# Performance work log

Measured on AMD Instinct MI355X. Metric: run time of the kernel, lower is better.

Reference implementation:

```python
import jax, jax.numpy as jnp
import numpy as np

B, D, H, W, C = 8, 4, 56, 56, 128
HEADS = 4
WD, WH, WW = 2, 7, 7
SD, SH, SW = 1, 3, 3
N = WD * WH * WW            # tokens per window = 98
NW = (D // WD) * (H // WH) * (W // WW)  # windows per sample = 128
SCALE = (C // HEADS) ** -0.5
EPS = 1e-5


def _rel_pos_index():
    coords = np.stack(np.meshgrid(np.arange(WD), np.arange(WH), np.arange(WW), indexing='ij'))
    coords = coords.reshape(3, -1)                    # (3, N)
    rel = (coords[:, :, None] - coords[:, None, :]).transpose(1, 2, 0)  # (N, N, 3)
    rel[:, :, 0] += WD - 1
    rel[:, :, 1] += WH - 1
    rel[:, :, 2] += WW - 1
    rel[:, :, 0] *= (2 * WH - 1) * (2 * WW - 1)
    rel[:, :, 1] *= (2 * WW - 1)
    return rel.sum(-1)                                # (N, N) int

REL_IDX = jnp.asarray(_rel_pos_index())


def _np_window_partition(x, wd, wh, ww):
    b, d, h, w, c = x.shape
    x = x.reshape(b, d // wd, wd, h // wh, wh, w // ww, ww, c)
    return x.transpose(0, 1, 3, 5, 2, 4, 6, 7).reshape(-1, wd * wh * ww, c)


def _attn_mask():
    img = np.zeros((1, D, H, W, 1), np.float32)
    cnt = 0
    for ds in (slice(None, -WD), slice(-WD, -SD), slice(-SD, None)):
        for hs in (slice(None, -WH), slice(-WH, -SH), slice(-SH, None)):
            for ws in (slice(None, -WW), slice(-WW, -SW), slice(-SW, None)):
                img[:, ds, hs, ws, :] = cnt
                cnt += 1
    mw = _np_window_partition(img, WD, WH, WW)[..., 0]         # (nW, N)
    m = mw[:, None, :] - mw[:, :, None]                        # (nW, N, N)
    return jnp.asarray(np.where(m != 0, -100.0, 0.0).astype(np.float32))

ATTN_MASK = _attn_mask()  # (nW, N, N)


def window_partition(x):
    b = x.shape[0]
    x = x.reshape(b, D // WD, WD, H // WH, WH, W // WW, WW, C)
    return x.transpose(0, 1, 3, 5, 2, 4, 6, 7).reshape(-1, N, C)


def window_reverse(wins, b):
    x = wins.reshape(b, D // WD, H // WH, W // WW, WD, WH, WW, C)
    return x.transpose(0, 1, 4, 2, 5, 3, 6, 7).reshape(b, D, H, W, C)


def layernorm(x, g, b):
    mu = jnp.mean(x, axis=-1, keepdims=True)
    var = jnp.mean(jnp.square(x - mu), axis=-1, keepdims=True)
    return (x - mu) / jnp.sqrt(var + EPS) * g + b


def swin_block(x, norm1_g, norm1_b, qkv_w, qkv_b, rpb_table, proj_w, proj_b,
               norm2_g, norm2_b, fc1_w, fc1_b, fc2_w, fc2_b):
    shortcut = x
    h1 = layernorm(x, norm1_g, norm1_b)
    # cyclic shift (pad amounts are 0 for these dims)
    shifted = jnp.roll(h1, (-SD, -SH, -SW), axis=(1, 2, 3))
    xw = window_partition(shifted)                    # (B*nW, N, C)
    Bn = xw.shape[0]
    qkv = (xw @ qkv_w + qkv_b).reshape(Bn, N, 3, HEADS, C // HEADS)
    qkv = qkv.transpose(2, 0, 3, 1, 4)                # (3, Bn, h, N, c)
    q, k, v = qkv[0], qkv[1], qkv[2]
    attn = jnp.einsum('bhnc,bhmc->bhnm', q * SCALE, k)
    bias = rpb_table[REL_IDX].transpose(2, 0, 1)      # (h, N, N)
    attn = attn + bias[None]
    attn = attn.reshape(B, NW, HEADS, N, N) + ATTN_MASK[None, :, None]
    attn = jax.nn.softmax(attn.reshape(Bn, HEADS, N, N), axis=-1)
    out = jnp.einsum('bhnm,bhmc->bhnc', attn, v)
    out = out.transpose(0, 2, 1, 3).reshape(Bn, N, C)
    out = out @ proj_w + proj_b
    xr = window_reverse(out, B)
    xr = jnp.roll(xr, (SD, SH, SW), axis=(1, 2, 3))
    x1 = shortcut + xr
    h2 = layernorm(x1, norm2_g, norm2_b)
    mlp = jax.nn.gelu(h2 @ fc1_w + fc1_b, approximate=False) @ fc2_w + fc2_b
    return x1 + mlp


def setup_inputs() -> dict:
    key = jax.random.key(0)
    ks = jax.random.split(key, 6)
    s = 0.02
    return {
        'x': jax.random.normal(ks[0], (B, D, H, W, C), jnp.float32),
        'norm1_g': jnp.ones((C,), jnp.float32),
        'norm1_b': jnp.zeros((C,), jnp.float32),
        'qkv_w': jax.random.normal(ks[1], (C, 3 * C), jnp.float32) * s,
        'qkv_b': jnp.zeros((3 * C,), jnp.float32),
        'rpb_table': jax.random.normal(ks[2], ((2 * WD - 1) * (2 * WH - 1) * (2 * WW - 1), HEADS), jnp.float32) * s,
        'proj_w': jax.random.normal(ks[3], (C, C), jnp.float32) * s,
        'proj_b': jnp.zeros((C,), jnp.float32),
        'norm2_g': jnp.ones((C,), jnp.float32),
        'norm2_b': jnp.zeros((C,), jnp.float32),
        'fc1_w': jax.random.normal(ks[4], (C, 4 * C), jnp.float32) * s,
        'fc1_b': jnp.zeros((4 * C,), jnp.float32),
        'fc2_w': jax.random.normal(ks[5], (4 * C, C), jnp.float32) * s,
        'fc2_b': jnp.zeros((C,), jnp.float32),
    }


def reference(x, norm1_g, norm1_b, qkv_w, qkv_b, rpb_table, proj_w, proj_b,
              norm2_g, norm2_b, fc1_w, fc1_b, fc2_w, fc2_b):
    return swin_block(x, norm1_g, norm1_b, qkv_w, qkv_b, rpb_table, proj_w, proj_b,
                      norm2_g, norm2_b, fc1_w, fc1_b, fc2_w, fc2_b)
```

## Files before the change

kernel.cpp:

```cpp
#include <hip/hip_runtime.h>
#include <hip/hip_bf16.h>
#include <cstdint>
#include <cstddef>

using bf16 = __hip_bfloat16;
typedef __bf16 bf16x8 __attribute__((ext_vector_type(8)));
typedef float f32x4 __attribute__((ext_vector_type(4)));

#define DEV static __device__ __forceinline__

DEV bf16 f2b(float x) { return __float2bfloat16(x); }
DEV float b2f(bf16 x) { return __bfloat162float(x); }
DEV f32x4 mfma16(bf16x8 a, bf16x8 b, f32x4 c) {
    return __builtin_amdgcn_mfma_f32_16x16x32_bf16(a, b, c, 0, 0, 0);
}
DEV float gelu_f(float x) {
    float u2 = x * x;
    float u = x * (0.7978845608028654f + 0.0356774081363001f * u2);
    float s = 1.f / (1.f + __expf(-2.f * u));
    return x * s;
}
DEV void gload16(const bf16* g, bf16* l) {
    __builtin_amdgcn_global_load_lds(
        (const __attribute__((address_space(1))) unsigned int*)g,
        (__attribute__((address_space(3))) unsigned int*)l, 16, 0, 0);
}

constexpr int NTOK = 98;
constexpr int BNWIN = 1024;
constexpr int MTOT = BNWIN * NTOK;
constexpr float SCALE = 0.17677669529663687f;
constexpr float EPS = 1e-5f;

__global__ __launch_bounds__(256) void k_prep(const float* __restrict__ qkv_w,
        const float* __restrict__ proj_w, const float* __restrict__ fc1_w,
        const float* __restrict__ fc2_w, const float* __restrict__ rpb,
        bf16* __restrict__ QWs, bf16* __restrict__ PW,
        bf16* __restrict__ W1, bf16* __restrict__ W2, float* __restrict__ BT) {
    int tid = blockIdx.x * 256 + threadIdx.x;
    int stride = gridDim.x * 256;
    for (int i = tid; i < 384 * 128; i += stride) {
        int t = i >> 13, r = (i >> 7) & 63, kswz = i & 127;
        int k = kswz ^ ((r & 7) << 3);
        QWs[i] = f2b(qkv_w[(size_t)k * 384 + t * 64 + r]);
    }
    for (int i = tid; i < 128 * 128; i += stride) {
        int n = i >> 7, k = i & 127;
        PW[i] = f2b(proj_w[k * 128 + n]);
    }
    for (int i = tid; i < 512 * 128; i += stride) {
        int t = i >> 13, r = (i >> 7) & 63, kswz = i & 127;
        int k = kswz ^ ((r & 7) << 3);
        W1[i] = f2b(fc1_w[(size_t)k * 512 + t * 64 + r]);
    }
    for (int i = tid; i < 512 * 128; i += stride) {
        int t = i >> 13, c = (i >> 6) & 127, kswz = i & 63;
        int kk = kswz ^ ((c & 7) << 3);
        W2[i] = f2b(fc2_w[(size_t)(t * 64 + kk) * 128 + c]);
    }
    for (int i = tid; i < 4 * 98 * 98; i += stride) {
        int h = i / 9604, r = i - h * 9604;
        int ii = r / 98, jj = r - ii * 98;
        int di = ii >= 49, ri = ii - di * 49, hi = ri / 7, wi = ri - hi * 7;
        int dj = jj >= 49, rj = jj - dj * 49, hj = rj / 7, wj = rj - hj * 7;
        int bidx = (di - dj + 1) * 169 + (hi - hj + 6) * 13 + (wi - wj + 6);
        BT[i] = rpb[bidx * 4 + h];
    }
}

__global__ __launch_bounds__(256) void k_qkvln(const float* __restrict__ x,
        const float* __restrict__ g, const float* __restrict__ be,
        const bf16* __restrict__ QWs, const float* __restrict__ bias,
        bf16* __restrict__ out) {
    __shared__ __align__(16) bf16 As[64 * 136];
    __shared__ __align__(16) bf16 Bt[64 * 128];
    int tid = threadIdx.x;
    int row0 = blockIdx.x * 64;
    int wave = tid >> 6, lane = tid & 63;
    int lrow = lane & 15, kg8 = (lane >> 4) * 8, g4 = (lane >> 4) * 4;
    int swzq = (lrow & 7) << 3;

    #pragma unroll
    for (int p = 0; p < 4; ++p) {
        int vi = tid + p * 256;
        int row = vi >> 4, cg = vi & 15;
        int r = row0 + row;
        int bn = r / 98, n = r - bn * 98;
        int b = bn >> 7, wr = bn & 127;
        int dB = wr >> 6, hB = (wr >> 3) & 7, wB = wr & 7;
        int dd = (n >= 49), rem = n - dd * 49;
        int hh = rem / 7, ww = rem - hh * 7;
        int dp = dB * 2 + dd, hp = hB * 7 + hh, wp = wB * 7 + ww;
        int ds = (dp + 1) & 3;
        int hs = hp + 3; if (hs >= 56) hs -= 56;
        int wsv = wp + 3; if (wsv >= 56) wsv -= 56;
        size_t src = ((size_t)((b * 4 + ds) * 56 + hs) * 56 + wsv) * 128 + cg * 8;
        float4 v0 = *(const float4*)&x[src];
        float4 v1 = *(const float4*)&x[src + 4];
        float s = v0.x + v0.y + v0.z + v0.w + v1.x + v1.y + v1.z + v1.w;
        float sq = v0.x*v0.x + v0.y*v0.y + v0.z*v0.z + v0.w*v0.w
                 + v1.x*v1.x + v1.y*v1.y + v1.z*v1.z + v1.w*v1.w;
        #pragma unroll
        for (int m = 1; m < 16; m <<= 1) { s += __shfl_xor(s, m); sq += __shfl_xor(sq, m); }
        float mean = s * (1.f / 128.f);
        float var = sq * (1.f / 128.f) - mean * mean;
        float rstd = rsqrtf(var + EPS);
        float4 g0 = *(const float4*)&g[cg * 8], g1 = *(const float4*)&g[cg * 8 + 4];
        float4 e0 = *(const float4*)&be[cg * 8], e1 = *(const float4*)&be[cg * 8 + 4];
        union { bf16x8 v8; bf16 h[8]; } o;
        o.h[0] = f2b((v0.x - mean) * rstd * g0.x + e0.x);
        o.h[1] = f2b((v0.y - mean) * rstd * g0.y + e0.y);
        o.h[2] = f2b((v0.z - mean) * rstd * g0.z + e0.z);
        o.h[3] = f2b((v0.w - mean) * rstd * g0.w + e0.w);
        o.h[4] = f2b((v1.x - mean) * rstd * g1.x + e1.x);
        o.h[5] = f2b((v1.y - mean) * rstd * g1.y + e1.y);
        o.h[6] = f2b((v1.z - mean) * rstd * g1.z + e1.z);
        o.h[7] = f2b((v1.w - mean) * rstd * g1.w + e1.w);
        *(bf16x8*)&As[row * 136 + cg * 8] = o.v8;
    }
    __syncthreads();

    bf16x8 a1[4];
    #pragma unroll
    for (int ksi = 0; ksi < 4; ++ksi)
        a1[ksi] = *(const bf16x8*)&As[(wave * 16 + lrow) * 136 + ksi * 32 + kg8];

    for (int c6 = 0; c6 < 6; ++c6) {
        const bf16* Bg = QWs + c6 * 8192;
        #pragma unroll
        for (int j = 0; j < 4; ++j) {
            int chunk = wave * 4 + j;
            gload16(Bg + chunk * 512 + lane * 8, Bt + chunk * 512);
        }
        __syncthreads();

        f32x4 acc[4] = {};
        #pragma unroll
        for (int ksi = 0; ksi < 4; ++ksi) {
            int k0 = ksi * 32 + kg8;
            #pragma unroll
            for (int ct = 0; ct < 4; ++ct) {
                bf16x8 bb = *(const bf16x8*)&Bt[(ct * 16 + lrow) * 128 + (k0 ^ swzq)];
                acc[ct] = mfma16(a1[ksi], bb, acc[ct]);
            }
        }
        #pragma unroll
        for (int ct = 0; ct < 4; ++ct) {
            int gcol = c6 * 64 + ct * 16 + lrow;
            float bv = bias[gcol];
            #pragma unroll
            for (int r2 = 0; r2 < 4; ++r2) {
                int grow = row0 + wave * 16 + g4 + r2;
                out[(size_t)grow * 384 + gcol] = f2b(acc[ct][r2] + bv);
            }
        }
        __syncthreads();
    }
}

__global__ __launch_bounds__(256) void k_attn(const bf16* __restrict__ qkv,
        const float* __restrict__ BT, bf16* __restrict__ aout) {
    __shared__ __align__(16) bf16 qs[112 * 40];
    __shared__ __align__(16) bf16 ksm[112 * 40];
    __shared__ __align__(16) bf16 vt[32 * 136];
    __shared__ __align__(16) bf16 ps[64 * 136];
    __shared__ signed char trg[112];

    int tid = threadIdx.x;
    int bn = blockIdx.x, h = blockIdx.y;
    int wrw = bn & 127;
    int dB = wrw >> 6, hB = (wrw >> 3) & 7, wB = wrw & 7;

    {
        uint32_t* z1 = (uint32_t*)qs;
        uint32_t* z2 = (uint32_t*)ksm;
        for (int i = tid; i < 2240; i += 256) { z1[i] = 0u; z2[i] = 0u; }
        uint32_t* z3 = (uint32_t*)vt;
        for (int i = tid; i < 2176; i += 256) z3[i] = 0u;
        uint32_t* z4 = (uint32_t*)ps;
        for (int i = tid; i < 4352; i += 256) z4[i] = 0u;
    }
    if (tid < 112) {
        int n = tid < 98 ? tid : 97;
        int dd = n >= 49, rem = n - dd * 49;
        int hh = rem / 7, ww2 = rem - hh * 7;
        int dp = dB * 2 + dd, hp = hB * 7 + hh, wp = wB * 7 + ww2;
        int rd = dp < 2 ? 0 : (dp == 2 ? 1 : 2);
        int rh = hp < 49 ? 0 : (hp < 53 ? 1 : 2);
        int rw = wp < 49 ? 0 : (wp < 53 ? 1 : 2);
        trg[tid] = (signed char)(rd * 9 + rh * 3 + rw);
    }
    __syncthreads();
    const size_t base = (size_t)bn * 98 * 384 + h * 32;
    for (int ch = tid; ch < 1176; ch += 256) {
        int mat = ch / 392;
        int rem = ch - mat * 392;
        int row = rem >> 2, cg = rem & 3;
        uint4 v = *(const uint4*)&qkv[base + (size_t)row * 384 + mat * 128 + cg * 8];
        if (mat == 0)      *(uint4*)&qs[row * 40 + cg * 8] = v;
        else if (mat == 1) *(uint4*)&ksm[row * 40 + cg * 8] = v;
        else {
            const bf16* pv = (const bf16*)&v;
            #pragma unroll
            for (int j = 0; j < 8; ++j) vt[(cg * 8 + j) * 136 + row] = pv[j];
        }
    }
    __syncthreads();

    int wave = tid >> 6, lane = tid & 63;
    int lrow = lane & 15, kg8 = (lane >> 4) * 8, g4 = (lane >> 4) * 4;

    for (int rt = wave; rt < 7; rt += 4) {
        f32x4 sacc[7];
        bf16x8 qa = *(const bf16x8*)&qs[(rt * 16 + lrow) * 40 + kg8];
        #pragma unroll
        for (int ct = 0; ct < 7; ++ct) {
            bf16x8 kb = *(const bf16x8*)&ksm[(ct * 16 + lrow) * 40 + kg8];
            f32x4 z = {};
            sacc[ct] = mfma16(qa, kb, z);
        }
        #pragma unroll
        for (int r2 = 0; r2 < 4; ++r2) {
            int grow = rt * 16 + g4 + r2;
            int mi = grow < 98 ? grow : 97;
            int mrg = trg[mi];
            const float* btrow = &BT[((size_t)h * 98 + mi) * 98];
            float val[7];
            float mx = -1e30f;
            #pragma unroll
            for (int ct = 0; ct < 7; ++ct) {
                int jc = ct * 16 + lrow;
                int jj = jc < 98 ? jc : 97;
                float bias = btrow[jj];
                float mv = (mrg != (int)trg[jj]) ? -100.f : 0.f;
                float v = sacc[ct][r2] * SCALE + bias + mv;
                if (jc >= 98) v = -1e30f;
                val[ct] = v;
                mx = fmaxf(mx, v);
            }
            #pragma unroll
            for (int m = 1; m < 16; m <<= 1) mx = fmaxf(mx, __shfl_xor(mx, m));
            float sum = 0.f;
            #pragma unroll
            for (int ct = 0; ct < 7; ++ct) { val[ct] = __expf(val[ct] - mx); sum += val[ct]; }
            #pragma unroll
            for (int m = 1; m < 16; m <<= 1) sum += __shfl_xor(sum, m);
            float inv = 1.f / sum;
            #pragma unroll
            for (int ct = 0; ct < 7; ++ct)
                ps[(wave * 16 + g4 + r2) * 136 + ct * 16 + lrow] = f2b(val[ct] * inv);
        }
        #pragma unroll
        for (int ct = 0; ct < 2; ++ct) {
            f32x4 oacc = {};
            #pragma unroll
            for (int ksi = 0; ksi < 4; ++ksi) {
                bf16x8 pa = *(const bf16x8*)&ps[(wave * 16 + lrow) * 136 + ksi * 32 + kg8];
                bf16x8 vb = *(const bf16x8*)&vt[(ct * 16 + lrow) * 136 + ksi * 32 + kg8];
                oacc = mfma16(pa, vb, oacc);
            }
            #pragma unroll
            for (int r2 = 0; r2 < 4; ++r2) {
                int grow = rt * 16 + g4 + r2;
                if (grow < 98)
                    aout[((size_t)bn * 98 + grow) * 128 + h * 32 + ct * 16 + lrow] =
                        f2b(oacc[r2]);
            }
        }
    }
}

__global__ __launch_bounds__(256) void k_proj(const bf16* __restrict__ A,
        const bf16* __restrict__ PW, const float* __restrict__ pb,
        const float* __restrict__ x, const float* __restrict__ g2,
        const float* __restrict__ be2,
        bf16* __restrict__ x1, bf16* __restrict__ h2) {
    __shared__ __align__(16) bf16 As[64 * 136];
    __shared__ __align__(16) bf16 Bt[128 * 136];
    int tid = threadIdx.x;
    int row0 = blockIdx.x * 64;
    #pragma unroll
    for (int p = 0; p < 4; ++p) {
        int vi = tid + p * 256;
        int row = vi >> 4, cg = vi & 15;
        *(uint4*)&As[row * 136 + cg * 8] =
            *(const uint4*)&A[(size_t)(row0 + row) * 128 + cg * 8];
    }
    #pragma unroll
    for (int p = 0; p < 8; ++p) {
        int vi = tid + p * 256;
        int row = vi >> 4, cg = vi & 15;
        *(uint4*)&Bt[row * 136 + cg * 8] =
            *(const uint4*)&PW[(size_t)row * 128 + cg * 8];
    }
    __syncthreads();
    int wave = tid >> 6, lane = tid & 63;
    int lrow = lane & 15, kg8 = (lane >> 4) * 8, g4 = (lane >> 4) * 4;
    f32x4 acc[8] = {};
    #pragma unroll
    for (int ksi = 0; ksi < 4; ++ksi) {
        bf16x8 a = *(const bf16x8*)&As[(wave * 16 + lrow) * 136 + ksi * 32 + kg8];
        #pragma unroll
        for (int ct = 0; ct < 8; ++ct) {
            bf16x8 bb = *(const bf16x8*)&Bt[(ct * 16 + lrow) * 136 + ksi * 32 + kg8];
            acc[ct] = mfma16(a, bb, acc[ct]);
        }
    }
    #pragma unroll
    for (int r2 = 0; r2 < 4; ++r2) {
        int rwin = row0 + wave * 16 + g4 + r2;
        int bn = rwin / 98, n = rwin - bn * 98;
        int b = bn >> 7, wr2 = bn & 127;
        int dB = wr2 >> 6, hB = (wr2 >> 3) & 7, wB = wr2 & 7;
        int dd = n >= 49, rem = n - dd * 49;
        int hh = rem / 7, ww2 = rem - hh * 7;
        int dp = dB * 2 + dd, hp = hB * 7 + hh, wp = wB * 7 + ww2;
        int d2 = (dp + 1) & 3;
        int hv = hp + 3; if (hv >= 56) hv -= 56;
        int wv = wp + 3; if (wv >= 56) wv -= 56;
        size_t dst = ((size_t)(b * 4 + d2) * 56 + hv) * 56 + wv;
        float vals[8], s = 0.f, sq = 0.f;
        #pragma unroll
        for (int ct = 0; ct < 8; ++ct) {
            int col = ct * 16 + lrow;
            float v = acc[ct][r2] + pb[col] + x[dst * 128 + col];
            vals[ct] = v; s += v; sq += v * v;
        }
        #pragma unroll
        for (int m = 1; m < 16; m <<= 1) { s += __shfl_xor(s, m); sq += __shfl_xor(sq, m); }
        float mean = s * (1.f / 128.f);
        float var = sq * (1.f / 128.f) - mean * mean;
        float rstd = rsqrtf(var + EPS);
        #pragma unroll
        for (int ct = 0; ct < 8; ++ct) {
            int col = ct * 16 + lrow;
            x1[dst * 128 + col] = f2b(vals[ct]);
            h2[dst * 128 + col] = f2b((vals[ct] - mean) * rstd * g2[col] + be2[col]);
        }
    }
}

__global__ __launch_bounds__(512) void k_mlp(const bf16* __restrict__ h2,
        const bf16* __restrict__ W1s, const float* __restrict__ b1,
        const bf16* __restrict__ W2s, const float* __restrict__ b2v,
        const bf16* __restrict__ x1, float* __restrict__ out) {
    __shared__ __align__(16) bf16 W1b[8192];
    __shared__ __align__(16) bf16 W2b[8192];
    __shared__ __align__(16) bf16 Ts[128 * 72];
    int tid = threadIdx.x;
    int row0 = blockIdx.x * 128;
    int wave = tid >> 6, lane = tid & 63;
    int lrow = lane & 15, kg8 = (lane >> 4) * 8, g4 = (lane >> 4) * 4;
    int swz = (lrow & 7) << 3;

    bf16x8 a1[4];
    const bf16* arow = &h2[(size_t)(row0 + wave * 16 + lrow) * 128];
    #pragma unroll
    for (int ksi = 0; ksi < 4; ++ksi)
        a1[ksi] = *(const bf16x8*)&arow[ksi * 32 + kg8];

    f32x4 oacc[8] = {};
    for (int hc = 0; hc < 8; ++hc) {
        const bf16* W1g = W1s + hc * 8192;
        const bf16* W2g = W2s + hc * 8192;
        #pragma unroll
        for (int j = 0; j < 4; ++j) {
            int chunk = wave + j * 8;
            if (chunk < 16) gload16(W1g + chunk * 512 + lane * 8, W1b + chunk * 512);
            else            gload16(W2g + (chunk - 16) * 512 + lane * 8, W2b + (chunk - 16) * 512);
        }
        __syncthreads();

        f32x4 tacc[4] = {};
        #pragma unroll
        for (int ksi = 0; ksi < 4; ++ksi) {
            int k0 = ksi * 32 + kg8;
            #pragma unroll
            for (int ct = 0; ct < 4; ++ct) {
                bf16x8 bb = *(const bf16x8*)&W1b[(ct * 16 + lrow) * 128 + (k0 ^ swz)];
                tacc[ct] = mfma16(a1[ksi], bb, tacc[ct]);
            }
        }
        #pragma unroll
        for (int ct = 0; ct < 4; ++ct) {
            int hcol = hc * 64 + ct * 16 + lrow;
            float bb = b1[hcol];
            #pragma unroll
            for (int r2 = 0; r2 < 4; ++r2) {
                float t = gelu_f(tacc[ct][r2] + bb);
                Ts[(wave * 16 + g4 + r2) * 72 + ct * 16 + lrow] = f2b(t);
            }
        }
        #pragma unroll
        for (int ksi = 0; ksi < 2; ++ksi) {
            int k0 = ksi * 32 + kg8;
            bf16x8 a = *(const bf16x8*)&Ts[(wave * 16 + lrow) * 72 + k0];
            #pragma unroll
            for (int ct = 0; ct < 8; ++ct) {
                bf16x8 bb = *(const bf16x8*)&W2b[(ct * 16 + lrow) * 64 + (k0 ^ swz)];
                oacc[ct] = mfma16(a, bb, oacc[ct]);
            }
        }
        __syncthreads();
    }
    #pragma unroll
    for (int ct = 0; ct < 8; ++ct) {
        int col = ct * 16 + lrow;
        float bb = b2v[col];
        #pragma unroll
        for (int r2 = 0; r2 < 4; ++r2) {
            size_t grow = (size_t)row0 + wave * 16 + g4 + r2;
            out[grow * 128 + col] = oacc[ct][r2] + bb + b2f(x1[grow * 128 + col]);
        }
    }
}

extern "C" void kernel_launch(void* const* d_in, const int* in_sizes, int n_in,
                              void* d_out, int out_size, void* d_ws, size_t ws_size,
                              hipStream_t stream) {
    (void)in_sizes; (void)n_in; (void)out_size; (void)ws_size;
    const float* x      = (const float*)d_in[0];
    const float* n1g    = (const float*)d_in[1];
    const float* n1b    = (const float*)d_in[2];
    const float* qkv_w  = (const float*)d_in[3];
    const float* qkv_b  = (const float*)d_in[4];
    const float* rpb    = (const float*)d_in[5];
    const float* proj_w = (const float*)d_in[6];
    const float* proj_b = (const float*)d_in[7];
    const float* n2g    = (const float*)d_in[8];
    const float* n2b    = (const float*)d_in[9];
    const float* fc1_w  = (const float*)d_in[10];
    const float* fc1_b  = (const float*)d_in[11];
    const float* fc2_w  = (const float*)d_in[12];
    const float* fc2_b  = (const float*)d_in[13];
    float* outp = (float*)d_out;

    char* ws = (char*)d_ws;
    constexpr size_t S = (size_t)MTOT * 128 * 2;
    bf16*  qkvbuf = (bf16*)(ws + S);
    bf16*  aout   = (bf16*)ws;
    bf16*  x1     = (bf16*)(ws + S);
    bf16*  h2     = (bf16*)(ws + 3 * S);
    char* wp_ = ws + 4 * S;
    bf16*  QWs = (bf16*)wp_;
    bf16*  PW  = (bf16*)(wp_ + 98304);
    bf16*  W1s = (bf16*)(wp_ + 98304 + 32768);
    bf16*  W2s = (bf16*)(wp_ + 98304 + 32768 + 131072);
    float* BTb = (float*)(wp_ + 98304 + 32768 + 131072 + 131072);

    k_prep <<<192, 256, 0, stream>>>(qkv_w, proj_w, fc1_w, fc2_w, rpb, QWs, PW, W1s, W2s, BTb);
    k_qkvln<<<MTOT / 64, 256, 0, stream>>>(x, n1g, n1b, QWs, qkv_b, qkvbuf);
    k_attn <<<dim3(BNWIN, 4), 256, 0, stream>>>(qkvbuf, BTb, aout);
    k_proj <<<MTOT / 64, 256, 0, stream>>>(aout, PW, proj_b, x, n2g, n2b, x1, h2);
    k_mlp  <<<MTOT / 128, 512, 0, stream>>>(h2, W1s, fc1_b, W2s, fc2_b, x1, outp);
}
```

Measured before the change: 197.6 us.

## Switch MLP kernel to 32x32x16 MFMA with 4 waves of 32 rows each

Rewrites the fused MLP kernel to use 32x32x16 bf16 MFMA tiles instead of 16x16x32, with each of 4 waves owning 32 rows rather than 8 waves owning 16. This raises per-wave arithmetic intensity and cuts LDS B-fragment reads per MFMA flop. Block size drops from 512 to 256 threads with a 3-blocks-per-CU launch bound. The cost is more accumulator registers per wave and fewer waves to hide latency. The weight-chunk loading and the swizzle are reindexed to match.

```diff
diff --git a/kernel.cpp b/kernel.cpp
--- a/kernel.cpp
+++ b/kernel.cpp
@@ -6,6 +6,7 @@
 using bf16 = __hip_bfloat16;
 typedef __bf16 bf16x8 __attribute__((ext_vector_type(8)));
 typedef float f32x4 __attribute__((ext_vector_type(4)));
+typedef float f32x16 __attribute__((ext_vector_type(16)));
 
 #define DEV static __device__ __forceinline__
 
@@ -13,6 +14,9 @@
 DEV float b2f(bf16 x) { return __bfloat162float(x); }
 DEV f32x4 mfma16(bf16x8 a, bf16x8 b, f32x4 c) {
     return __builtin_amdgcn_mfma_f32_16x16x32_bf16(a, b, c, 0, 0, 0);
+}
+DEV f32x16 mfma32(bf16x8 a, bf16x8 b, f32x16 c) {
+    return __builtin_amdgcn_mfma_f32_32x32x16_bf16(a, b, c, 0, 0, 0);
 }
 DEV float gelu_f(float x) {
     float u2 = x * x;
@@ -340,7 +344,7 @@
     }
 }
 
-__global__ __launch_bounds__(512) void k_mlp(const bf16* __restrict__ h2,
+__global__ __launch_bounds__(256, 3) void k_mlp(const bf16* __restrict__ h2,
         const bf16* __restrict__ W1s, const float* __restrict__ b1,
         const bf16* __restrict__ W2s, const float* __restrict__ b2v,
         const bf16* __restrict__ x1, float* __restrict__ out) {
@@ -350,67 +354,68 @@
     int tid = threadIdx.x;
     int row0 = blockIdx.x * 128;
     int wave = tid >> 6, lane = tid & 63;
-    int lrow = lane & 15, kg8 = (lane >> 4) * 8, g4 = (lane >> 4) * 4;
-    int swz = (lrow & 7) << 3;
-
-    bf16x8 a1[4];
-    const bf16* arow = &h2[(size_t)(row0 + wave * 16 + lrow) * 128];
-    #pragma unroll
-    for (int ksi = 0; ksi < 4; ++ksi)
-        a1[ksi] = *(const bf16x8*)&arow[ksi * 32 + kg8];
-
-    f32x4 oacc[8] = {};
-    for (int hc = 0; hc < 8; ++hc) {
-        const bf16* W1g = W1s + hc * 8192;
-        const bf16* W2g = W2s + hc * 8192;
-        #pragma unroll
-        for (int j = 0; j < 4; ++j) {
-            int chunk = wave + j * 8;
+    int l31 = lane & 31, hi = lane >> 5;
+    int swz = (lane & 7) << 3;
+
+    bf16x8 a1[8];
+    const bf16* arow = &h2[(size_t)(row0 + wave * 32 + l31) * 128 + hi * 8];
+    #pragma unroll
+    for (int ks = 0; ks < 8; ++ks)
+        a1[ks] = *(const bf16x8*)&arow[ks * 16];
+
+    f32x16 oacc[4] = {};
+    for (int q = 0; q < 8; ++q) {
+        const bf16* W1g = W1s + q * 8192;
+        const bf16* W2g = W2s + q * 8192;
+        #pragma unroll
+        for (int j = 0; j < 8; ++j) {
+            int chunk = wave * 8 + j;
             if (chunk < 16) gload16(W1g + chunk * 512 + lane * 8, W1b + chunk * 512);
             else            gload16(W2g + (chunk - 16) * 512 + lane * 8, W2b + (chunk - 16) * 512);
         }
         __syncthreads();
 
-        f32x4 tacc[4] = {};
-        #pragma unroll
-        for (int ksi = 0; ksi < 4; ++ksi) {
-            int k0 = ksi * 32 + kg8;
-            #pragma unroll
-            for (int ct = 0; ct < 4; ++ct) {
-                bf16x8 bb = *(const bf16x8*)&W1b[(ct * 16 + lrow) * 128 + (k0 ^ swz)];
-                tacc[ct] = mfma16(a1[ksi], bb, tacc[ct]);
-            }
-        }
-        #pragma unroll
-        for (int ct = 0; ct < 4; ++ct) {
-            int hcol = hc * 64 + ct * 16 + lrow;
-            float bb = b1[hcol];
-            #pragma unroll
-            for (int r2 = 0; r2 < 4; ++r2) {
-                float t = gelu_f(tacc[ct][r2] + bb);
-                Ts[(wave * 16 + g4 + r2) * 72 + ct * 16 + lrow] = f2b(t);
-            }
-        }
-        #pragma unroll
-        for (int ksi = 0; ksi < 2; ++ksi) {
-            int k0 = ksi * 32 + kg8;
-            bf16x8 a = *(const bf16x8*)&Ts[(wave * 16 + lrow) * 72 + k0];
-            #pragma unroll
-            for (int ct = 0; ct < 8; ++ct) {
-                bf16x8 bb = *(const bf16x8*)&W2b[(ct * 16 + lrow) * 64 + (k0 ^ swz)];
-                oacc[ct] = mfma16(a, bb, oacc[ct]);
+        f32x16 tacc[2] = {};
+        #pragma unroll
+        for (int ks = 0; ks < 8; ++ks) {
+            int k0 = ks * 16 + hi * 8;
+            #pragma unroll
+            for (int ht = 0; ht < 2; ++ht) {
+                bf16x8 bb = *(const bf16x8*)&W1b[(ht * 32 + l31) * 128 + (k0 ^ swz)];
+                tacc[ht] = mfma32(a1[ks], bb, tacc[ht]);
+            }
+        }
+        #pragma unroll
+        for (int ht = 0; ht < 2; ++ht) {
+            float bbv = b1[q * 64 + ht * 32 + l31];
+            #pragma unroll
+            for (int r = 0; r < 16; ++r) {
+                int row = (r & 3) + 8 * (r >> 2) + 4 * hi;
+                Ts[(wave * 32 + row) * 72 + ht * 32 + l31] =
+                    f2b(gelu_f(tacc[ht][r] + bbv));
+            }
+        }
+        #pragma unroll
+        for (int ks = 0; ks < 4; ++ks) {
+            int k0 = ks * 16 + hi * 8;
+            bf16x8 a = *(const bf16x8*)&Ts[(wave * 32 + l31) * 72 + k0];
+            #pragma unroll
+            for (int ot = 0; ot < 4; ++ot) {
+                bf16x8 bb = *(const bf16x8*)&W2b[(ot * 32 + l31) * 64 + (k0 ^ swz)];
+                oacc[ot] = mfma32(a, bb, oacc[ot]);
             }
         }
         __syncthreads();
     }
     #pragma unroll
-    for (int ct = 0; ct < 8; ++ct) {
-        int col = ct * 16 + lrow;
-        float bb = b2v[col];
-        #pragma unroll
-        for (int r2 = 0; r2 < 4; ++r2) {
-            size_t grow = (size_t)row0 + wave * 16 + g4 + r2;
-            out[grow * 128 + col] = oacc[ct][r2] + bb + b2f(x1[grow * 128 + col]);
+    for (int ot = 0; ot < 4; ++ot) {
+        int col = ot * 32 + l31;
+        float bbv = b2v[col];
+        #pragma unroll
+        for (int r = 0; r < 16; ++r) {
+            int row = (r & 3) + 8 * (r >> 2) + 4 * hi;
+            size_t grow = (size_t)row0 + wave * 32 + row;
+            out[grow * 128 + col] = oacc[ot][r] + bbv + b2f(x1[grow * 128 + col]);
         }
     }
 }
@@ -452,5 +457,5 @@
     k_qkvln<<<MTOT / 64, 256, 0, stream>>>(x, n1g, n1b, QWs, qkv_b, qkvbuf);
     k_attn <<<dim3(BNWIN, 4), 256, 0, stream>>>(qkvbuf, BTb, aout);
     k_proj <<<MTOT / 64, 256, 0, stream>>>(aout, PW, proj_b, x, n2g, n2b, x1, h2);
-    k_mlp  <<<MTOT / 128, 512, 0, stream>>>(h2, W1s, fc1_b, W2s, fc2_b, x1, outp);
-}
+    k_mlp  <<<MTOT / 128, 256, 0, stream>>>(h2, W1s, fc1_b, W2s, fc2_b, x1, outp);
+}
```

Result: faster. 192.7 us (-2.5%).
